# Kernel optimization log

Hardware: AMD Instinct MI355X
Metric: run time of the kernel (lower is better)

The kernel has to match this reference:

```python
import jax, jax.numpy as jnp
import numpy as np

EPS = 1e-6


def setup_inputs() -> dict:
    key = jax.random.key(0)
    k1, k2, k3 = jax.random.split(key, 3)
    h, w, K = 480, 640, 21
    n = h * w
    segmentation = jax.random.uniform(k1, (n, K), dtype=jnp.float32)  # per-pixel plane probs in (0,1)
    prob = jax.random.uniform(k2, (n, 1), dtype=jnp.float32)
    gt_instance = jax.random.randint(k3, (21, h, w), 0, 2, dtype=jnp.int32)  # binary GT masks
    return {
        "segmentation": segmentation,
        "prob": prob,
        "gt_instance": gt_instance,
        "gt_plane_num": 20,
    }


def reference(segmentation, prob, gt_instance, gt_plane_num):
    # segmentation: (N, K) probabilities; gt_instance: (21, h, w) binary; gt_plane_num: python int
    n, k = segmentation.shape
    # (G, N) float masks for the first gt_plane_num GT instances
    gi = gt_instance[:gt_plane_num].reshape(gt_plane_num, -1).astype(jnp.float32)
    seg = segmentation.T  # (K, N)
    log_p = jnp.log(seg + EPS)        # (K, N)
    log_1p = jnp.log(1.0 - seg + EPS)  # (K, N)
    # mean over pixels of -(gi*log_p + (1-gi)*log_1p), expressed as two GEMMs
    # instead of materializing the (K, G, N) broadcast tensor:
    # ce[k, g] = -( sum_n log_p[k,n]*gi[g,n] + sum_n log_1p[k,n]*(1-gi[g,n]) ) / N
    inv_n = jnp.float32(1.0 / n)
    ce = -(log_p @ gi.T + log_1p @ (1.0 - gi).T) * inv_n  # (K, G)
    matching = jnp.argmin(ce, axis=1, keepdims=True)  # (K, 1) int
    return matching
```

## Files before the change

### kernel.cpp

```cpp
#include <hip/hip_runtime.h>

#define EPSF 1e-6f
#define TPB 256
#define KMAXC 21
#define NGR 21
#define RW 72
#define SLICE (KMAXC * RW)
#define TBL 1024
#define NREP 8
#define SUMS_FLOATS (NREP * TBL)

typedef float  f32x4  __attribute__((ext_vector_type(4)));
typedef float  f32x16 __attribute__((ext_vector_type(16)));
typedef __bf16 bf16x8 __attribute__((ext_vector_type(8)));
typedef __bf16 bf16x4 __attribute__((ext_vector_type(4)));

struct GroupRegs { f32x4 s[6]; int4 g[6]; };

__device__ __forceinline__ void issue_loads(const float* __restrict__ seg,
                                            const int* __restrict__ gt,
                                            int N, int GROWS, int p0, int lane,
                                            GroupRegs& r) {
    const f32x4* s4 = (const f32x4*)(seg + (size_t)p0 * KMAXC);
    #pragma unroll
    for (int q = 0; q < 6; ++q) {
        const int i4 = lane + (q << 6);
        f32x4 v = {0.5f, 0.5f, 0.5f, 0.5f};
        if (i4 < 336) v = s4[i4];
        r.s[q] = v;
    }
    #pragma unroll
    for (int q = 0; q < 6; ++q) {
        const int i4 = lane + (q << 6);
        int4 gv = {0, 0, 0, 0};
        if (i4 < 336) {
            int row = i4 >> 4;
            row = (row < GROWS) ? row : (GROWS - 1);
            gv = *(const int4*)(gt + (size_t)row * N + p0 + ((i4 & 15) << 2));
        }
        r.g[q] = gv;
    }
}

__device__ __forceinline__ void scatter_group(__bf16* dl, __bf16* ml, int lane,
                                              const GroupRegs& r) {
    #pragma unroll
    for (int q = 0; q < 6; ++q) {
        const int i4 = lane + (q << 6);
        if (i4 < 336) {
            const int lin = i4 << 2;
            int pix = lin / KMAXC;
            int k   = lin - pix * KMAXC;
            #pragma unroll
            for (int c = 0; c < 4; ++c) {
                const float s = r.s[q][c];
                const float dd = __log2f(s + EPSF) - __log2f(1.0f - s + EPSF);
                dl[k * RW + pix] = (__bf16)dd;
                if (++k == KMAXC) { k = 0; ++pix; }
            }
            const int row = i4 >> 4;
            bf16x4 mv;
            mv[0] = (__bf16)(float)(r.g[q].x != 0);
            mv[1] = (__bf16)(float)(r.g[q].y != 0);
            mv[2] = (__bf16)(float)(r.g[q].z != 0);
            mv[3] = (__bf16)(float)(r.g[q].w != 0);
            *(bf16x4*)(ml + row * RW + ((i4 & 15) << 2)) = mv;
        }
    }
}

__device__ __forceinline__ void mfma_group(const __bf16* dl, const __bf16* ml,
                                           int lane, int K, f32x16& acc) {
    const int r31  = lane & 31;
    const int rowA = (r31 < K)   ? r31 : (K - 1);
    const int rowB = (r31 < NGR) ? r31 : (NGR - 1);
    const int off  = (lane >> 5) << 3;
    const __bf16* pa = dl + rowA * RW + off;
    const __bf16* pb = ml + rowB * RW + off;
    #pragma unroll
    for (int i = 0; i < 4; ++i) {
        const bf16x8 af = *(const bf16x8*)(pa + i * 16);
        const bf16x8 bf = *(const bf16x8*)(pb + i * 16);
        acc = __builtin_amdgcn_mfma_f32_32x32x16_bf16(af, bf, acc, 0, 0, 0);
    }
}

__device__ __forceinline__ void generic_group(const float* __restrict__ seg,
                                              const int* __restrict__ gt,
                                              __bf16* dl, __bf16* ml, int lane,
                                              int N, int K, int GROWS, int p0) {
    for (int i = lane; i < K * 64; i += 64) {
        const int pix = i / K, k = i - pix * K;
        const float s = (p0 + pix < N) ? seg[(size_t)(p0 + pix) * K + k] : 0.5f;
        const float dd = __log2f(s + EPSF) - __log2f(1.0f - s + EPSF);
        if (k < KMAXC) dl[k * RW + pix] = (__bf16)dd;
    }
    for (int i = lane; i < NGR * 64; i += 64) {
        const int row = i >> 6, c = i & 63;
        int val = 0;
        if (row < GROWS && p0 + c < N) val = (gt[(size_t)row * N + p0 + c] != 0);
        ml[row * RW + c] = (__bf16)(float)val;
    }
}

__global__ __launch_bounds__(TPB) void msk_zero(float* __restrict__ sums) {
    const int idx = blockIdx.x * TPB + threadIdx.x;
    if (idx < SUMS_FLOATS)
        __hip_atomic_store(&sums[idx], 0.0f, __ATOMIC_RELAXED,
                           __HIP_MEMORY_SCOPE_AGENT);
}

__global__ __launch_bounds__(TPB) void msk_main(
    const float* __restrict__ seg,
    const int* __restrict__ gt,
    const int* __restrict__ gpn,
    float* __restrict__ sums,
    int N, int K, int GROWS, int NGROUP, int NBLK)
{
    const int G = *gpn;
    const int tid  = threadIdx.x;
    const int lane = tid & 63;
    const int wv   = tid >> 6;

    __shared__ union {
        __bf16 stage[4][2][SLICE];
        float  red[4 * TBL];
    } u;

    f32x16 acc = {};
    __bf16* dl = u.stage[wv][0];
    __bf16* ml = u.stage[wv][1];

    const int W  = NBLK * 4;
    const int gw = (int)blockIdx.x * 4 + wv;

    if (K == KMAXC) {
        const int g0 = gw, g1 = gw + W;
        const bool f0 = (g0 < NGROUP) && ((g0 << 6) + 64 <= N);
        const bool f1 = (g1 < NGROUP) && ((g1 << 6) + 64 <= N);
        GroupRegs r0, r1;
        if (f0) issue_loads(seg, gt, N, GROWS, g0 << 6, lane, r0);
        if (f1) issue_loads(seg, gt, N, GROWS, g1 << 6, lane, r1);
        if (f0) { scatter_group(dl, ml, lane, r0); mfma_group(dl, ml, lane, K, acc); }
        if (f1) { scatter_group(dl, ml, lane, r1); mfma_group(dl, ml, lane, K, acc); }
        if (g0 < NGROUP && !f0) {
            generic_group(seg, gt, dl, ml, lane, N, K, GROWS, g0 << 6);
            mfma_group(dl, ml, lane, K, acc);
        }
        if (g1 < NGROUP && !f1) {
            generic_group(seg, gt, dl, ml, lane, N, K, GROWS, g1 << 6);
            mfma_group(dl, ml, lane, K, acc);
        }
        for (int gid = gw + 2 * W; gid < NGROUP; gid += W) {
            const int p0 = gid << 6;
            if (p0 + 64 <= N) {
                GroupRegs r;
                issue_loads(seg, gt, N, GROWS, p0, lane, r);
                scatter_group(dl, ml, lane, r);
            } else {
                generic_group(seg, gt, dl, ml, lane, N, K, GROWS, p0);
            }
            mfma_group(dl, ml, lane, K, acc);
        }
    } else {
        for (int gid = gw; gid < NGROUP; gid += W) {
            generic_group(seg, gt, dl, ml, lane, N, K, GROWS, gid << 6);
            mfma_group(dl, ml, lane, K, acc);
        }
    }

    __syncthreads();
    {
        const int col = lane & 31;
        const int rhi = (lane >> 5) << 2;
        #pragma unroll
        for (int r = 0; r < 16; ++r) {
            const int row = (r & 3) + ((r >> 2) << 3) + rhi;
            u.red[wv * TBL + row * 32 + col] = acc[r];
        }
    }
    __syncthreads();

    {
        float* stbl = sums + (size_t)(blockIdx.x & (NREP - 1)) * TBL;
        #pragma unroll
        for (int q = 0; q < TBL / TPB; ++q) {
            const int cell = q * TPB + tid;
            const float v = u.red[cell] + u.red[TBL + cell]
                          + u.red[2 * TBL + cell] + u.red[3 * TBL + cell];
            const int row = cell >> 5, col = cell & 31;
            if (row < K && col < G) atomicAdd(&stbl[cell], v);
        }
    }
}

__global__ __launch_bounds__(TPB) void msk_final(
    const float* __restrict__ sums,
    const int* __restrict__ gpn,
    int* __restrict__ out,
    int K)
{
    const int G = *gpn;
    const int tid = threadIdx.x;
    __shared__ float A[KMAXC * 32 + 32];

    const int NC = K * 32;
    for (int c = tid; c < NC; c += TPB) {
        float v = 0.f;
        #pragma unroll
        for (int r = 0; r < NREP; ++r)
            v += __hip_atomic_load(&sums[(size_t)r * TBL + c], __ATOMIC_RELAXED,
                                   __HIP_MEMORY_SCOPE_AGENT);
        A[c] = v;
    }
    __syncthreads();

    if (tid < K) {
        const int GG = (G < 32) ? G : 32;
        float bv; int bg = 0;
        if (GG > 0) {
            bv = A[tid * 32];
            for (int g = 1; g < GG; ++g) {
                const float v = A[tid * 32 + g];
                if (v > bv) { bv = v; bg = g; }
            }
        }
        out[tid] = bg;
    }
}

extern "C" void kernel_launch(void* const* d_in, const int* in_sizes, int n_in,
                              void* d_out, int out_size, void* d_ws, size_t ws_size,
                              hipStream_t stream) {
    const float* seg = (const float*)d_in[0];
    const int* gt  = (const int*)d_in[2];
    const int* gpn = (const int*)d_in[3];

    const int N = in_sizes[1];
    const int K = in_sizes[0] / N;
    const int GROWS = in_sizes[2] / N;
    const int NGROUP = (N + 63) >> 6;

    int NBLK = 600;
    const int minb = (NGROUP + 3) >> 2;
    if (NBLK > minb) NBLK = minb;
    if (NBLK < 1) NBLK = 1;

    msk_zero <<<SUMS_FLOATS / TPB, TPB, 0, stream>>>((float*)d_ws);
    msk_main <<<NBLK, TPB, 0, stream>>>(seg, gt, gpn, (float*)d_ws,
                                        N, K, GROWS, NGROUP, NBLK);
    msk_final<<<1, TPB, 0, stream>>>((const float*)d_ws, gpn, (int*)d_out, K);
}
```

Measured before the change: 25.69 us.

## Replace atomic partial sums with per-block tables and parallel final reduction

Drops the zeroing kernel and the atomicAdd reduction into 8 replicated tables. Each main block now writes its own full partial table with plain stores, and the final kernel runs one block per plane (K blocks of 512 threads) to sum all block tables in parallel before doing the argmax. The main grid size is also raised to up to 1200 blocks, capped by workspace size. This removes a launch and atomic contention, at the cost of more workspace traffic and a larger final reduction.

```diff
diff --git a/kernel.cpp b/kernel.cpp
--- a/kernel.cpp
+++ b/kernel.cpp
@@ -7,8 +7,7 @@
 #define RW 72
 #define SLICE (KMAXC * RW)
 #define TBL 1024
-#define NREP 8
-#define SUMS_FLOATS (NREP * TBL)
+#define MAXBLK 1200
 
 typedef float  f32x4  __attribute__((ext_vector_type(4)));
 typedef float  f32x16 __attribute__((ext_vector_type(16)));
@@ -103,21 +102,12 @@
     }
 }
 
-__global__ __launch_bounds__(TPB) void msk_zero(float* __restrict__ sums) {
-    const int idx = blockIdx.x * TPB + threadIdx.x;
-    if (idx < SUMS_FLOATS)
-        __hip_atomic_store(&sums[idx], 0.0f, __ATOMIC_RELAXED,
-                           __HIP_MEMORY_SCOPE_AGENT);
-}
-
 __global__ __launch_bounds__(TPB) void msk_main(
     const float* __restrict__ seg,
     const int* __restrict__ gt,
-    const int* __restrict__ gpn,
     float* __restrict__ sums,
     int N, int K, int GROWS, int NGROUP, int NBLK)
 {
-    const int G = *gpn;
     const int tid  = threadIdx.x;
     const int lane = tid & 63;
     const int wv   = tid >> 6;
@@ -182,50 +172,71 @@
     __syncthreads();
 
     {
-        float* stbl = sums + (size_t)(blockIdx.x & (NREP - 1)) * TBL;
+        float* stbl = sums + (size_t)blockIdx.x * TBL;
         #pragma unroll
         for (int q = 0; q < TBL / TPB; ++q) {
             const int cell = q * TPB + tid;
             const float v = u.red[cell] + u.red[TBL + cell]
                           + u.red[2 * TBL + cell] + u.red[3 * TBL + cell];
-            const int row = cell >> 5, col = cell & 31;
-            if (row < K && col < G) atomicAdd(&stbl[cell], v);
-        }
-    }
-}
-
-__global__ __launch_bounds__(TPB) void msk_final(
+            __hip_atomic_store(&stbl[cell], v, __ATOMIC_RELAXED,
+                               __HIP_MEMORY_SCOPE_AGENT);
+        }
+    }
+}
+
+__global__ __launch_bounds__(512) void msk_final(
     const float* __restrict__ sums,
     const int* __restrict__ gpn,
     int* __restrict__ out,
-    int K)
+    int K, int NBLK)
 {
     const int G = *gpn;
+    const int k = blockIdx.x;
     const int tid = threadIdx.x;
-    __shared__ float A[KMAXC * 32 + 32];
-
-    const int NC = K * 32;
-    for (int c = tid; c < NC; c += TPB) {
-        float v = 0.f;
+    const int col = tid & 31;
+    const int grp = tid >> 5;
+
+    float v0 = 0.f, v1 = 0.f, v2 = 0.f, v3 = 0.f;
+    const size_t base = (size_t)k * 32 + col;
+    int tbl = grp;
+    for (; tbl + 48 < NBLK; tbl += 64) {
+        v0 += __hip_atomic_load(&sums[(size_t)(tbl     ) * TBL + base],
+                                __ATOMIC_RELAXED, __HIP_MEMORY_SCOPE_AGENT);
+        v1 += __hip_atomic_load(&sums[(size_t)(tbl + 16) * TBL + base],
+                                __ATOMIC_RELAXED, __HIP_MEMORY_SCOPE_AGENT);
+        v2 += __hip_atomic_load(&sums[(size_t)(tbl + 32) * TBL + base],
+                                __ATOMIC_RELAXED, __HIP_MEMORY_SCOPE_AGENT);
+        v3 += __hip_atomic_load(&sums[(size_t)(tbl + 48) * TBL + base],
+                                __ATOMIC_RELAXED, __HIP_MEMORY_SCOPE_AGENT);
+    }
+    for (; tbl < NBLK; tbl += 16)
+        v0 += __hip_atomic_load(&sums[(size_t)tbl * TBL + base],
+                                __ATOMIC_RELAXED, __HIP_MEMORY_SCOPE_AGENT);
+    const float v = (v0 + v1) + (v2 + v3);
+
+    __shared__ float P[16][33];
+    __shared__ float A[32];
+    P[grp][col] = v;
+    __syncthreads();
+    if (tid < 32) {
+        float s = 0.f;
         #pragma unroll
-        for (int r = 0; r < NREP; ++r)
-            v += __hip_atomic_load(&sums[(size_t)r * TBL + c], __ATOMIC_RELAXED,
-                                   __HIP_MEMORY_SCOPE_AGENT);
-        A[c] = v;
-    }
-    __syncthreads();
-
-    if (tid < K) {
+        for (int g2 = 0; g2 < 16; ++g2) s += P[g2][tid];
+        A[tid] = s;
+    }
+    __syncthreads();
+
+    if (tid == 0) {
         const int GG = (G < 32) ? G : 32;
         float bv; int bg = 0;
         if (GG > 0) {
-            bv = A[tid * 32];
+            bv = A[0];
             for (int g = 1; g < GG; ++g) {
-                const float v = A[tid * 32 + g];
-                if (v > bv) { bv = v; bg = g; }
+                const float vv = A[g];
+                if (vv > bv) { bv = vv; bg = g; }
             }
         }
-        out[tid] = bg;
+        out[k] = bg;
     }
 }
 
@@ -241,13 +252,15 @@
     const int GROWS = in_sizes[2] / N;
     const int NGROUP = (N + 63) >> 6;
 
-    int NBLK = 600;
+    int NBLK = MAXBLK;
     const int minb = (NGROUP + 3) >> 2;
     if (NBLK > minb) NBLK = minb;
+    const long long wcap = (long long)(ws_size / (TBL * sizeof(float)));
+    if (NBLK > wcap) NBLK = (int)wcap;
     if (NBLK < 1) NBLK = 1;
 
-    msk_zero <<<SUMS_FLOATS / TPB, TPB, 0, stream>>>((float*)d_ws);
-    msk_main <<<NBLK, TPB, 0, stream>>>(seg, gt, gpn, (float*)d_ws,
+    msk_main <<<NBLK, TPB, 0, stream>>>(seg, gt, (float*)d_ws,
                                         N, K, GROWS, NGROUP, NBLK);
-    msk_final<<<1, TPB, 0, stream>>>((const float*)d_ws, gpn, (int*)d_out, K);
-}
+    msk_final<<<K, 512, 0, stream>>>((const float*)d_ws, gpn, (int*)d_out,
+                                     K, NBLK);
+}
```

New measurement: 25.21 us. Within noise of the previous version (-1.8%).
